# Kernel optimization log

Measured on AMD Instinct MI355X. Metric: run time of the kernel, lower is better.

Reference implementation:

```python
import jax, jax.numpy as jnp
import numpy as np

B, T, C = 4, 2048, 1024
N_HEADS = 16
HEAD_DIM = C // N_HEADS


def rotary_embedding(seq_len, dim, dtype=jnp.float32):
    pos = jnp.arange(seq_len, dtype=dtype)[:, None]
    i = jnp.arange(0, dim, 2, dtype=dtype)[None, :]
    theta = pos / jnp.power(10000.0, i / dim)
    return jnp.cos(theta), jnp.sin(theta)


def apply_rotary(x, cos, sin):
    # x: [B, T, H, D]; cos/sin: [T, D//2]
    d = x.shape[-1]
    x1, x2 = x[..., : d // 2], x[..., d // 2 :]
    rotated = jnp.concatenate([-x2, x1], axis=-1)
    cos = jnp.concatenate([cos, cos], axis=-1)[None, :, None, :]
    sin = jnp.concatenate([sin, sin], axis=-1)[None, :, None, :]
    return x * cos + rotated * sin


def setup_inputs() -> dict:
    key = jax.random.key(0)
    k1, k2, k3 = jax.random.split(key, 3)
    x = jax.random.normal(k1, (B, T, C), dtype=jnp.float32)
    # lecun_normal-ish init scale
    w_qkv = jax.random.normal(k2, (C, 3 * C), dtype=jnp.float32) / np.sqrt(C)
    w_out = jax.random.normal(k3, (C, C), dtype=jnp.float32) / np.sqrt(C)
    return {"x": x, "w_qkv": w_qkv, "w_out": w_out}


def reference(x, w_qkv, w_out):
    b, t, c = x.shape
    qkv = jnp.einsum("btc,cd->btd", x, w_qkv)
    q, k, v = jnp.split(qkv, 3, axis=-1)
    q = q.reshape(b, t, N_HEADS, HEAD_DIM)
    k = k.reshape(b, t, N_HEADS, HEAD_DIM)
    v = v.reshape(b, t, N_HEADS, HEAD_DIM)
    cos, sin = rotary_embedding(t, HEAD_DIM, dtype=x.dtype)
    q = apply_rotary(q, cos, sin)
    k = apply_rotary(k, cos, sin)
    scale = jnp.sqrt(jnp.asarray(HEAD_DIM, dtype=x.dtype))
    # scores: [B, H, T, T]
    attn = jnp.einsum("bqhd,bkhd->bhqk", q, k) / scale
    mask = jnp.tril(jnp.ones((t, t), dtype=jnp.bool_))
    attn = jnp.where(mask[None, None, :, :], attn, jnp.asarray(-1e9, dtype=x.dtype))
    attn = jax.nn.softmax(attn, axis=-1)
    out = jnp.einsum("bhqk,bkhd->bqhd", attn, v).reshape(b, t, c)
    return jnp.einsum("btc,cd->btd", out, w_out)
```

## Files before the change

### kernel.cpp

```cpp
#include <hip/hip_runtime.h>
#include <stdint.h>

#define DEVI __device__ __forceinline__

typedef unsigned short ushort_t;
typedef __bf16 bf16x8 __attribute__((ext_vector_type(8)));
typedef float f32x4 __attribute__((ext_vector_type(4)));
typedef unsigned short ushort8 __attribute__((ext_vector_type(8)));
typedef unsigned short u16x4 __attribute__((ext_vector_type(4)));
typedef short s16x4 __attribute__((ext_vector_type(4)));

#define BB 4
#define TT 2048
#define CC 1024
#define NH 16
#define HD 64
#define MM (BB*TT)

DEVI ushort_t f2bf(float f) {
    __bf16 h = (__bf16)f;
    return __builtin_bit_cast(ushort_t, h);
}

typedef const __attribute__((address_space(1))) unsigned int guint_t;
typedef __attribute__((address_space(3))) unsigned int luint_t;

DEVI void gl2lds16(const void* g, void* lds) {
    __builtin_amdgcn_global_load_lds((guint_t*)(uintptr_t)g,
                                     (luint_t*)(unsigned int)(uintptr_t)lds,
                                     16, 0, 0);
}

template <int N> DEVI void waitvm() {
    static_assert(N == 0 || N == 4, "unsupported vmcnt literal");
    if constexpr (N == 0)      asm volatile("s_waitcnt vmcnt(0)" ::: "memory");
    else if constexpr (N == 4) asm volatile("s_waitcnt vmcnt(4)" ::: "memory");
}

#define BARF() do { asm volatile("" ::: "memory"); \
                    __builtin_amdgcn_s_barrier(); \
                    asm volatile("" ::: "memory"); } while (0)
#define LGK0() asm volatile("s_waitcnt lgkmcnt(0)" ::: "memory")

__global__ void cvt_f32_bf16(const float* __restrict__ in,
                             ushort_t* __restrict__ out) {
    int i = blockIdx.x * 256 + threadIdx.x;
    const float4* p = (const float4*)in + (size_t)i * 2;
    float4 a = p[0], b = p[1];
    ushort8 r;
    r[0] = f2bf(a.x); r[1] = f2bf(a.y); r[2] = f2bf(a.z); r[3] = f2bf(a.w);
    r[4] = f2bf(b.x); r[5] = f2bf(b.y); r[6] = f2bf(b.z); r[7] = f2bf(b.w);
    *(ushort8*)(out + (size_t)i * 8) = r;
}

__global__ void transpose_f2b(const float* __restrict__ in,
                              ushort_t* __restrict__ out, int R, int Cc) {
    __shared__ ushort_t tile[32][33];
    int bx = blockIdx.x * 32;
    int by = blockIdx.y * 32;
    int tx = threadIdx.x & 31, ty = threadIdx.x >> 5;
    #pragma unroll
    for (int i = 0; i < 4; i++) {
        int r = ty * 4 + i;
        tile[r][tx] = f2bf(in[(size_t)(by + r) * Cc + bx + tx]);
    }
    __syncthreads();
    #pragma unroll
    for (int i = 0; i < 4; i++) {
        int r = ty * 4 + i;
        out[(size_t)(bx + r) * R + by + tx] = tile[tx][r];
    }
}

__global__ void rope_table(float2* __restrict__ tab) {
    int i = blockIdx.x * 256 + threadIdx.x;
    int t = i >> 5, j = i & 31;
    float inv = exp2f((float)j * -0.41524101186092029f);
    float theta = (float)t * inv;
    float s, c;
    sincosf(theta, &s, &c);
    tab[i] = make_float2(c, s);
}

template <int MODE>
__global__ __launch_bounds__(512, 2) void gemm_bt(
    const ushort_t* __restrict__ A, const ushort_t* __restrict__ Bt,
    float* __restrict__ CoutF,
    ushort_t* __restrict__ Qb, ushort_t* __restrict__ Kb, ushort_t* __restrict__ VbT,
    const float2* __restrict__ rope, int M, int N, int Kd) {
    constexpr int NK = CC / 64;
    (void)M;

    __shared__ __attribute__((aligned(16))) ushort_t As[2][256 * 64];
    __shared__ __attribute__((aligned(16))) ushort_t Bs[2][256 * 64];

    const int tid = threadIdx.x;
    const int w = tid >> 6, l = tid & 63;
    const int lane15 = l & 15, quad = l >> 4;
    const int wm = (w >> 2) * 128;
    const int wn = (w & 3) * 64;

    const int nbn = gridDim.x;
    const int nwg = nbn * gridDim.y;
    const int lid = blockIdx.y * nbn + blockIdx.x;
    const int sid = (lid & 7) * (nwg >> 3) + (lid >> 3);
    const int bn = sid % nbn, bm = sid / nbn;

    const int sr = tid >> 3;
    const int sc = tid & 7;
    const int srcswz = (sc ^ (sr & 7)) * 16;

    auto stA = [&](int buf, int t, int ln) {
        int gr = bm * 256 + ln * 64 + sr;
        size_t e;
        if constexpr (MODE == 2)
            e = (size_t)(gr >> 11) * 2097152 + (size_t)t * 131072
                + (size_t)(gr & (TT - 1)) * 64;
        else
            e = (size_t)gr * (size_t)Kd + (size_t)t * 64;
        gl2lds16((const char*)(A + e) + srcswz,
                 (char*)&As[buf][0] + ln * 8192 + tid * 16);
    };
    auto stB = [&](int buf, int t, int ln) {
        int gr = bn * 256 + ln * 64 + sr;
        size_t e = (size_t)gr * (size_t)Kd + (size_t)t * 64;
        gl2lds16((const char*)(Bt + e) + srcswz,
                 (char*)&Bs[buf][0] + ln * 8192 + tid * 16);
    };

    f32x4 acc[8][4];
    #pragma unroll
    for (int m = 0; m < 8; ++m)
        #pragma unroll
        for (int n = 0; n < 4; ++n)
            acc[m][n] = f32x4{0.f, 0.f, 0.f, 0.f};

    stA(0, 0, 0); stA(0, 0, 1); stA(0, 0, 2); stA(0, 0, 3);
    stB(0, 0, 0); stB(0, 0, 1); stB(0, 0, 2); stB(0, 0, 3);
    stB(1, 1, 0); stB(1, 1, 1); stB(1, 1, 2); stB(1, 1, 3);
    waitvm<4>();
    BARF();

    const int swz = (lane15 & 7) << 4;
    bf16x8 aR[4][2];
    bf16x8 bR[4][2];

#define LDA_H(P, MH)                                                          \
    { _Pragma("unroll") for (int i = 0; i < 4; ++i)                           \
      _Pragma("unroll") for (int kk = 0; kk < 2; ++kk)                        \
        aR[i][kk] = *(const bf16x8*)((const char*)&As[P][0] +                 \
            (wm + MH * 64 + i * 16 + lane15) * 128 +                          \
            ((kk * 64 + quad * 16) ^ swz)); }

#define LDB_H(P, NHF)                                                         \
    { _Pragma("unroll") for (int j = 0; j < 2; ++j)                           \
      _Pragma("unroll") for (int kk = 0; kk < 2; ++kk)                        \
        bR[NHF * 2 + j][kk] = *(const bf16x8*)((const char*)&Bs[P][0] +       \
            (wn + (NHF * 2 + j) * 16 + lane15) * 128 +                        \
            ((kk * 64 + quad * 16) ^ swz)); }

#define MFMA_Q(MH, NHF)                                                       \
    { __builtin_amdgcn_s_setprio(1);                                          \
      _Pragma("unroll") for (int kk = 0; kk < 2; ++kk)                        \
      _Pragma("unroll") for (int i = 0; i < 4; ++i)                           \
      _Pragma("unroll") for (int j = 0; j < 2; ++j)                           \
        acc[MH * 4 + i][NHF * 2 + j] =                                        \
            __builtin_amdgcn_mfma_f32_16x16x32_bf16(                          \
                aR[i][kk], bR[NHF * 2 + j][kk], acc[MH * 4 + i][NHF * 2 + j], \
                0, 0, 0);                                                     \
      __builtin_amdgcn_s_setprio(0); }

    for (int t = 0; t < NK; ++t) {
        const int p = t & 1;
        const bool s1 = (t + 1 < NK), s2 = (t + 2 < NK);
        LDA_H(p, 0);
        LDB_H(p, 0);
        if (s1) { stA(p ^ 1, t + 1, 0); stA(p ^ 1, t + 1, 1); }
        BARF(); LGK0();
        MFMA_Q(0, 0);
        BARF();
        LDB_H(p, 1);
        if (s1) { stA(p ^ 1, t + 1, 2); stA(p ^ 1, t + 1, 3); }
        BARF(); LGK0();
        MFMA_Q(0, 1);
        BARF();
        LDA_H(p, 1);
        if (s2) { stB(p, t + 2, 0); stB(p, t + 2, 1); }
        BARF(); LGK0();
        MFMA_Q(1, 1);
        BARF();
        if (s2) { stB(p, t + 2, 2); stB(p, t + 2, 3); }
        MFMA_Q(1, 0);
        if (s1) {
            if (s2) waitvm<4>();
            else    waitvm<0>();
            BARF();
        }
    }
#undef LDA_H
#undef LDB_H
#undef MFMA_Q

    if constexpr (MODE == 1) {
        const float SCQ = 0.125f * 1.4426950408889634f;
        const int colbase = bn * 256 + wn;
        const int seg = colbase >> 10;
        const int h = (colbase & 1023) >> 6;
        if (seg == 2) {
            __syncthreads();
            ushort_t* scr = ((w & 4) ? &Bs[0][0] : &As[0][0]) + (w & 3) * 2560;
            const int t0 = bm * 256 + wm;
            const int bq = t0 >> 11;
            const int tb = t0 & (TT - 1);
            const size_t obase = (size_t)(bq * NH + h) * (TT * HD);
            #pragma unroll
            for (int hp = 0; hp < 4; ++hp) {
                #pragma unroll
                for (int mp = 0; mp < 2; ++mp) {
                    int m = hp * 2 + mp;
                    #pragma unroll
                    for (int n = 0; n < 4; ++n) {
                        u16x4 v;
                        v[0] = f2bf(acc[m][n][0]);
                        v[1] = f2bf(acc[m][n][1]);
                        v[2] = f2bf(acc[m][n][2]);
                        v[3] = f2bf(acc[m][n][3]);
                        *(u16x4*)&scr[(n * 16 + lane15) * 40 +
                                      mp * 16 + quad * 4] = v;
                    }
                }
                LGK0();
                __builtin_amdgcn_sched_barrier(0);
                #pragma unroll
                for (int i = 0; i < 4; ++i) {
                    int dd = i * 16 + (l >> 2);
                    int tl = (l & 3) * 8;
                    ushort8 vv = *(const ushort8*)&scr[dd * 40 + tl];
                    *(ushort8*)(VbT + obase + (size_t)dd * TT +
                                tb + hp * 32 + tl) = vv;
                }
                if (hp < 3) { LGK0(); __builtin_amdgcn_sched_barrier(0); }
            }
        } else {
            ushort_t* dst = (seg == 0) ? Qb : Kb;
            #pragma unroll
            for (int m = 0; m < 8; ++m) {
                int row0 = bm * 256 + wm + m * 16 + quad * 4;
                #pragma unroll
                for (int r = 0; r < 4; ++r) {
                    int row = row0 + r;
                    int b = row >> 11, t = row & (TT - 1);
                    size_t ob = ((size_t)(b * NH + h) * TT + t) * HD;
                    #pragma unroll
                    for (int n = 0; n < 2; ++n) {
                        int j = n * 16 + lane15;
                        float2 cs = rope[t * 32 + j];
                        float x1 = acc[m][n][r];
                        float x2 = acc[m][n + 2][r];
                        float y1 = x1 * cs.x - x2 * cs.y;
                        float y2 = x2 * cs.x + x1 * cs.y;
                        if (seg == 0) { y1 *= SCQ; y2 *= SCQ; }
                        dst[ob + j]      = f2bf(y1);
                        dst[ob + 32 + j] = f2bf(y2);
                    }
                }
            }
        }
    } else {
        #pragma unroll
        for (int m = 0; m < 8; ++m) {
            #pragma unroll
            for (int r = 0; r < 4; ++r) {
                size_t rb = (size_t)(bm * 256 + wm + m * 16 + quad * 4 + r) * N
                            + bn * 256 + wn;
                #pragma unroll
                for (int n = 0; n < 4; ++n)
                    CoutF[rb + n * 16 + lane15] = acc[m][n][r];
            }
        }
    }
}

__global__ __launch_bounds__(512, 4) void attn_kernel(
    ushort_t* __restrict__ Qb, const ushort_t* __restrict__ Kb,
    const ushort_t* __restrict__ VbT) {
    __shared__ __attribute__((aligned(16))) ushort_t Ks[2][64 * 64];
    __shared__ __attribute__((aligned(16))) ushort_t Vs[2][64 * 64];

    const int tid = threadIdx.x;
    const int w = tid >> 6, l = tid & 63;
    const int lane15 = l & 15, quad = l >> 4;

    const int d = blockIdx.y * gridDim.x + blockIdx.x;
    const int xcd = d & 7, j = d >> 3;
    const int bh = xcd * 8 + (j & 7);
    const int qt = (int)((0x765489AB3210CDEFull >> (4 * (j >> 3))) & 15);
    const size_t base = (size_t)bh * (TT * HD);

    const int sr = tid >> 3;
    const int sd = (tid & 7) * 8;
    const int scol = (sd * 2) ^ ((sr & 7) << 4);
    const ushort_t* kgb = Kb  + base + (size_t)sr * HD + sd;
    const ushort_t* vgb = VbT + base + (size_t)sr * TT + sd;

    const int q0 = qt * 128;
    const int rbase = q0 + w * 16;
    const int ktmax = 2 * qt + 1;

    bf16x8 qf0, qf1;
    {
        const ushort_t* qp = Qb + base + (size_t)(rbase + lane15) * HD + quad * 8;
        qf0 = *(const bf16x8*)qp;
        qf1 = *(const bf16x8*)(qp + 32);
    }

    f32x4 o[4];
    #pragma unroll
    for (int nt = 0; nt < 4; nt++) o[nt] = f32x4{0.f, 0.f, 0.f, 0.f};
    f32x4 lacc = f32x4{0.f, 0.f, 0.f, 0.f};
    float mrow = -INFINITY;

    const s16x4 ONES = {(short)0x3F80, (short)0x3F80,
                        (short)0x3F80, (short)0x3F80};

    const int rsw = (lane15 & 7) << 4;

    ushort8 kr = *(const ushort8*)kgb;
    ushort8 vr = *(const ushort8*)vgb;
    *(ushort8*)((char*)&Ks[0][0] + sr * 128 + scol) = kr;
    *(ushort8*)((char*)&Vs[0][0] + sr * 128 + scol) = vr;
    kr = *(const ushort8*)(kgb + (size_t)64 * HD);
    vr = *(const ushort8*)(vgb + 64);
    __syncthreads();

    for (int kt = 0; kt <= ktmax; kt++) {
        const int buf = kt & 1;
        if (kt < ktmax) {
            *(ushort8*)((char*)&Ks[buf ^ 1][0] + sr * 128 + scol) = kr;
            *(ushort8*)((char*)&Vs[buf ^ 1][0] + sr * 128 + scol) = vr;
        }
        if (kt + 2 <= ktmax) {
            kr = *(const ushort8*)(kgb + (size_t)(kt + 2) * 64 * HD);
            vr = *(const ushort8*)(vgb + (size_t)(kt + 2) * 64);
        }

        if (kt * 64 <= rbase + 15) {
            f32x4 s[4];
            #pragma unroll
            for (int c = 0; c < 4; c++) {
                const char* krow = (const char*)&Ks[buf][0]
                                   + (c * 16 + lane15) * 128;
                bf16x8 k0 = *(const bf16x8*)(krow + ((quad * 16) ^ rsw));
                bf16x8 k1 = *(const bf16x8*)(krow + ((64 + quad * 16) ^ rsw));
                f32x4 z = f32x4{0.f, 0.f, 0.f, 0.f};
                z = __builtin_amdgcn_mfma_f32_16x16x32_bf16(k0, qf0, z, 0, 0, 0);
                s[c] = __builtin_amdgcn_mfma_f32_16x16x32_bf16(k1, qf1, z, 0, 0, 0);
            }

            const int qrow = rbase + lane15;
            if (kt * 64 + 63 > rbase) {
                #pragma unroll
                for (int c = 0; c < 4; c++)
                    #pragma unroll
                    for (int r = 0; r < 4; r++)
                        if (kt * 64 + c * 16 + quad * 4 + r > qrow) s[c][r] = -1e9f;
            }

            float a0 = fmaxf(fmaxf(s[0][0], s[0][1]), s[0][2]);
            float a1 = fmaxf(fmaxf(s[0][3], s[1][0]), s[1][1]);
            float a2 = fmaxf(fmaxf(s[1][2], s[1][3]), s[2][0]);
            float a3 = fmaxf(fmaxf(s[2][1], s[2][2]), s[2][3]);
            float a4 = fmaxf(fmaxf(s[3][0], s[3][1]), s[3][2]);
            float mt = fmaxf(fmaxf(a0, a1), a2);
            mt = fmaxf(fmaxf(mt, a3), fmaxf(a4, s[3][3]));

            if (!__all(mt - mrow <= 8.0f)) {
                float mf = fmaxf(mt, __shfl_xor(mt, 16, 64));
                mf = fmaxf(mf, __shfl_xor(mf, 32, 64));
                float mn = fmaxf(mrow, mf);
                float alpha = __builtin_amdgcn_exp2f(mrow - mn);
                mrow = mn;
                #pragma unroll
                for (int r = 0; r < 4; r++) {
                    float aO = __shfl(alpha, quad * 4 + r, 64);
                    #pragma unroll
                    for (int nt = 0; nt < 4; nt++) o[nt][r] *= aO;
                    lacc[r] *= aO;
                }
            }

            #pragma unroll
            for (int c = 0; c < 4; c++) {
                s16x4 pf;
                #pragma unroll
                for (int r = 0; r < 4; r++)
                    pf[r] = (short)f2bf(__builtin_amdgcn_exp2f(s[c][r] - mrow));
                lacc = __builtin_amdgcn_mfma_f32_16x16x16bf16_1k(
                    pf, ONES, lacc, 0, 0, 0);
                #pragma unroll
                for (int nt = 0; nt < 4; nt++) {
                    s16x4 vf = *(const s16x4*)((const char*)&Vs[buf][0] +
                        (nt * 16 + lane15) * 128 +
                        ((c * 32 + quad * 8) ^ rsw));
                    o[nt] = __builtin_amdgcn_mfma_f32_16x16x16bf16_1k(
                        pf, vf, o[nt], 0, 0, 0);
                }
            }
        }

        if (kt < ktmax) __syncthreads();
    }

    #pragma unroll
    for (int r = 0; r < 4; r++) {
        float lO = 1.0f / lacc[r];
        size_t rb = base + (size_t)(rbase + quad * 4 + r) * HD;
        #pragma unroll
        for (int nt = 0; nt < 4; nt++)
            Qb[rb + nt * 16 + lane15] = f2bf(o[nt][r] * lO);
    }
}

extern "C" void kernel_launch(void* const* d_in, const int* in_sizes, int n_in,
                              void* d_out, int out_size, void* d_ws, size_t ws_size,
                              hipStream_t stream) {
    const float* x    = (const float*)d_in[0];
    const float* wqkv = (const float*)d_in[1];
    const float* wout = (const float*)d_in[2];
    float* out = (float*)d_out;

    char* ws = (char*)d_ws;
    ushort_t* WqkvT = (ushort_t*)(ws);
    ushort_t* WoutT = (ushort_t*)(ws + 6291456);
    float2*   rope  = (float2*)  (ws + 8388608);
    ushort_t* Xb    = (ushort_t*)(ws + 8912896);
    ushort_t* Qb    = (ushort_t*)(ws + 8912896 + 16777216);
    ushort_t* Kb    = (ushort_t*)(ws + 8912896 + 2 * 16777216);
    ushort_t* VbT   = (ushort_t*)(ws + 8912896 + 3 * 16777216);

    cvt_f32_bf16<<<dim3(MM * CC / (256 * 8)), 256, 0, stream>>>(x, Xb);
    transpose_f2b<<<dim3(3 * CC / 32, CC / 32), 256, 0, stream>>>(wqkv, WqkvT, CC, 3 * CC);
    transpose_f2b<<<dim3(CC / 32, CC / 32), 256, 0, stream>>>(wout, WoutT, CC, CC);
    rope_table<<<dim3(256), 256, 0, stream>>>(rope);

    gemm_bt<1><<<dim3(3 * CC / 256, MM / 256), 512, 0, stream>>>(
        Xb, WqkvT, nullptr, Qb, Kb, VbT, rope, MM, 3 * CC, CC);

    attn_kernel<<<dim3(16, BB * NH), 512, 0, stream>>>(Qb, Kb, VbT);

    gemm_bt<2><<<dim3(CC / 256, MM / 256), 512, 0, stream>>>(
        Qb, WoutT, out, nullptr, nullptr, nullptr, nullptr, MM, CC, CC);
}
```

Before: 250.6 us.

## Fuse prep kernels and pair causal attention query tiles per block

Merges the four preprocessing launches (x conversion, two weight transposes, rope table) into one kernel that dispatches on block index, removing launch overhead. The attention kernel now launches half as many blocks, and each block processes two query tiles, qt=15-xq and qt=xq, one after the other. This gives every block the same amount of causal work, so block-level load imbalance from the triangular mask goes away. The cost is fewer concurrent blocks (512 instead of 1024), less parallelism, and an extra barrier between the two segments.

```diff
diff --git a/kernel.cpp b/kernel.cpp
--- a/kernel.cpp
+++ b/kernel.cpp
@@ -42,44 +42,53 @@
                     asm volatile("" ::: "memory"); } while (0)
 #define LGK0() asm volatile("s_waitcnt lgkmcnt(0)" ::: "memory")
 
-__global__ void cvt_f32_bf16(const float* __restrict__ in,
-                             ushort_t* __restrict__ out) {
-    int i = blockIdx.x * 256 + threadIdx.x;
-    const float4* p = (const float4*)in + (size_t)i * 2;
-    float4 a = p[0], b = p[1];
-    ushort8 r;
-    r[0] = f2bf(a.x); r[1] = f2bf(a.y); r[2] = f2bf(a.z); r[3] = f2bf(a.w);
-    r[4] = f2bf(b.x); r[5] = f2bf(b.y); r[6] = f2bf(b.z); r[7] = f2bf(b.w);
-    *(ushort8*)(out + (size_t)i * 8) = r;
-}
-
-__global__ void transpose_f2b(const float* __restrict__ in,
-                              ushort_t* __restrict__ out, int R, int Cc) {
+__global__ __launch_bounds__(256) void prep(
+    const float* __restrict__ x, ushort_t* __restrict__ Xb,
+    const float* __restrict__ wqkv, ushort_t* __restrict__ WqkvT,
+    const float* __restrict__ wout, ushort_t* __restrict__ WoutT,
+    float2* __restrict__ rope) {
     __shared__ ushort_t tile[32][33];
-    int bx = blockIdx.x * 32;
-    int by = blockIdx.y * 32;
-    int tx = threadIdx.x & 31, ty = threadIdx.x >> 5;
-    #pragma unroll
-    for (int i = 0; i < 4; i++) {
-        int r = ty * 4 + i;
-        tile[r][tx] = f2bf(in[(size_t)(by + r) * Cc + bx + tx]);
+    const int b = blockIdx.x, tid = threadIdx.x;
+    if (b < 4096) {
+        int i = b * 256 + tid;
+        const float4* p = (const float4*)x + (size_t)i * 2;
+        float4 a = p[0], c = p[1];
+        ushort8 r;
+        r[0] = f2bf(a.x); r[1] = f2bf(a.y); r[2] = f2bf(a.z); r[3] = f2bf(a.w);
+        r[4] = f2bf(c.x); r[5] = f2bf(c.y); r[6] = f2bf(c.z); r[7] = f2bf(c.w);
+        *(ushort8*)(Xb + (size_t)i * 8) = r;
+    } else if (b < 8192) {
+        const float* in; ushort_t* out; int Cc, bx, by;
+        if (b < 7168) {
+            int b2 = b - 4096;
+            in = wqkv; out = WqkvT; Cc = 3 * CC;
+            bx = (b2 % 96) * 32; by = (b2 / 96) * 32;
+        } else {
+            int b3 = b - 7168;
+            in = wout; out = WoutT; Cc = CC;
+            bx = (b3 & 31) * 32; by = (b3 >> 5) * 32;
+        }
+        int tx = tid & 31, ty = tid >> 5;
+        #pragma unroll
+        for (int i = 0; i < 4; i++) {
+            int r = ty * 4 + i;
+            tile[r][tx] = f2bf(in[(size_t)(by + r) * Cc + bx + tx]);
+        }
+        __syncthreads();
+        #pragma unroll
+        for (int i = 0; i < 4; i++) {
+            int r = ty * 4 + i;
+            out[(size_t)(bx + r) * CC + by + tx] = tile[tx][r];
+        }
+    } else {
+        int i = (b - 8192) * 256 + tid;
+        int t = i >> 5, jj = i & 31;
+        float inv = exp2f((float)jj * -0.41524101186092029f);
+        float theta = (float)t * inv;
+        float s, c;
+        sincosf(theta, &s, &c);
+        rope[i] = make_float2(c, s);
     }
-    __syncthreads();
-    #pragma unroll
-    for (int i = 0; i < 4; i++) {
-        int r = ty * 4 + i;
-        out[(size_t)(bx + r) * R + by + tx] = tile[tx][r];
-    }
-}
-
-__global__ void rope_table(float2* __restrict__ tab) {
-    int i = blockIdx.x * 256 + threadIdx.x;
-    int t = i >> 5, j = i & 31;
-    float inv = exp2f((float)j * -0.41524101186092029f);
-    float theta = (float)t * inv;
-    float s, c;
-    sincosf(theta, &s, &c);
-    tab[i] = make_float2(c, s);
 }
 
 template <int MODE>
@@ -294,7 +303,7 @@
     const int d = blockIdx.y * gridDim.x + blockIdx.x;
     const int xcd = d & 7, j = d >> 3;
     const int bh = xcd * 8 + (j & 7);
-    const int qt = (int)((0x765489AB3210CDEFull >> (4 * (j >> 3))) & 15);
+    const int xq = j >> 3;
     const size_t base = (size_t)bh * (TT * HD);
 
     const int sr = tid >> 3;
@@ -303,121 +312,128 @@
     const ushort_t* kgb = Kb  + base + (size_t)sr * HD + sd;
     const ushort_t* vgb = VbT + base + (size_t)sr * TT + sd;
 
-    const int q0 = qt * 128;
-    const int rbase = q0 + w * 16;
-    const int ktmax = 2 * qt + 1;
-
-    bf16x8 qf0, qf1;
-    {
-        const ushort_t* qp = Qb + base + (size_t)(rbase + lane15) * HD + quad * 8;
-        qf0 = *(const bf16x8*)qp;
-        qf1 = *(const bf16x8*)(qp + 32);
-    }
-
-    f32x4 o[4];
-    #pragma unroll
-    for (int nt = 0; nt < 4; nt++) o[nt] = f32x4{0.f, 0.f, 0.f, 0.f};
-    f32x4 lacc = f32x4{0.f, 0.f, 0.f, 0.f};
-    float mrow = -INFINITY;
-
+    const int rsw = (lane15 & 7) << 4;
     const s16x4 ONES = {(short)0x3F80, (short)0x3F80,
                         (short)0x3F80, (short)0x3F80};
 
-    const int rsw = (lane15 & 7) << 4;
-
-    ushort8 kr = *(const ushort8*)kgb;
-    ushort8 vr = *(const ushort8*)vgb;
-    *(ushort8*)((char*)&Ks[0][0] + sr * 128 + scol) = kr;
-    *(ushort8*)((char*)&Vs[0][0] + sr * 128 + scol) = vr;
-    kr = *(const ushort8*)(kgb + (size_t)64 * HD);
-    vr = *(const ushort8*)(vgb + 64);
-    __syncthreads();
-
-    for (int kt = 0; kt <= ktmax; kt++) {
-        const int buf = kt & 1;
-        if (kt < ktmax) {
-            *(ushort8*)((char*)&Ks[buf ^ 1][0] + sr * 128 + scol) = kr;
-            *(ushort8*)((char*)&Vs[buf ^ 1][0] + sr * 128 + scol) = vr;
-        }
-        if (kt + 2 <= ktmax) {
-            kr = *(const ushort8*)(kgb + (size_t)(kt + 2) * 64 * HD);
-            vr = *(const ushort8*)(vgb + (size_t)(kt + 2) * 64);
-        }
-
-        if (kt * 64 <= rbase + 15) {
-            f32x4 s[4];
+    #pragma unroll 1
+    for (int seg = 0; seg < 2; ++seg) {
+        const int qt = seg ? xq : 15 - xq;
+        const int q0 = qt * 128;
+        const int rbase = q0 + w * 16;
+        const int ktmax = 2 * qt + 1;
+
+        bf16x8 qf0, qf1;
+        {
+            const ushort_t* qp = Qb + base + (size_t)(rbase + lane15) * HD
+                                 + quad * 8;
+            qf0 = *(const bf16x8*)qp;
+            qf1 = *(const bf16x8*)(qp + 32);
+        }
+
+        f32x4 o[4];
+        #pragma unroll
+        for (int nt = 0; nt < 4; nt++) o[nt] = f32x4{0.f, 0.f, 0.f, 0.f};
+        f32x4 lacc = f32x4{0.f, 0.f, 0.f, 0.f};
+        float mrow = -INFINITY;
+
+        if (seg) __syncthreads();
+
+        ushort8 kr = *(const ushort8*)kgb;
+        ushort8 vr = *(const ushort8*)vgb;
+        *(ushort8*)((char*)&Ks[0][0] + sr * 128 + scol) = kr;
+        *(ushort8*)((char*)&Vs[0][0] + sr * 128 + scol) = vr;
+        kr = *(const ushort8*)(kgb + (size_t)64 * HD);
+        vr = *(const ushort8*)(vgb + 64);
+        __syncthreads();
+
+        for (int kt = 0; kt <= ktmax; kt++) {
+            const int buf = kt & 1;
+            if (kt < ktmax) {
+                *(ushort8*)((char*)&Ks[buf ^ 1][0] + sr * 128 + scol) = kr;
+                *(ushort8*)((char*)&Vs[buf ^ 1][0] + sr * 128 + scol) = vr;
+            }
+            if (kt + 2 <= ktmax) {
+                kr = *(const ushort8*)(kgb + (size_t)(kt + 2) * 64 * HD);
+                vr = *(const ushort8*)(vgb + (size_t)(kt + 2) * 64);
+            }
+
+            if (kt * 64 <= rbase + 15) {
+                f32x4 s[4];
+                #pragma unroll
+                for (int c = 0; c < 4; c++) {
+                    const char* krow = (const char*)&Ks[buf][0]
+                                       + (c * 16 + lane15) * 128;
+                    bf16x8 k0 = *(const bf16x8*)(krow + ((quad * 16) ^ rsw));
+                    bf16x8 k1 = *(const bf16x8*)(krow + ((64 + quad * 16) ^ rsw));
+                    f32x4 z = f32x4{0.f, 0.f, 0.f, 0.f};
+                    z = __builtin_amdgcn_mfma_f32_16x16x32_bf16(k0, qf0, z, 0, 0, 0);
+                    s[c] = __builtin_amdgcn_mfma_f32_16x16x32_bf16(k1, qf1, z, 0, 0, 0);
+                }
+
+                const int qrow = rbase + lane15;
+                if (kt * 64 + 63 > rbase) {
+                    #pragma unroll
+                    for (int c = 0; c < 4; c++)
+                        #pragma unroll
+                        for (int r = 0; r < 4; r++)
+                            if (kt * 64 + c * 16 + quad * 4 + r > qrow)
+                                s[c][r] = -1e9f;
+                }
+
+                float a0 = fmaxf(fmaxf(s[0][0], s[0][1]), s[0][2]);
+                float a1 = fmaxf(fmaxf(s[0][3], s[1][0]), s[1][1]);
+                float a2 = fmaxf(fmaxf(s[1][2], s[1][3]), s[2][0]);
+                float a3 = fmaxf(fmaxf(s[2][1], s[2][2]), s[2][3]);
+                float a4 = fmaxf(fmaxf(s[3][0], s[3][1]), s[3][2]);
+                float mt = fmaxf(fmaxf(a0, a1), a2);
+                mt = fmaxf(fmaxf(mt, a3), fmaxf(a4, s[3][3]));
+
+                if (!__all(mt - mrow <= 8.0f)) {
+                    float mf = fmaxf(mt, __shfl_xor(mt, 16, 64));
+                    mf = fmaxf(mf, __shfl_xor(mf, 32, 64));
+                    float mn = fmaxf(mrow, mf);
+                    float alpha = __builtin_amdgcn_exp2f(mrow - mn);
+                    mrow = mn;
+                    #pragma unroll
+                    for (int r = 0; r < 4; r++) {
+                        float aO = __shfl(alpha, quad * 4 + r, 64);
+                        #pragma unroll
+                        for (int nt = 0; nt < 4; nt++) o[nt][r] *= aO;
+                        lacc[r] *= aO;
+                    }
+                }
+
+                #pragma unroll
+                for (int c = 0; c < 4; c++) {
+                    s16x4 pf;
+                    #pragma unroll
+                    for (int r = 0; r < 4; r++)
+                        pf[r] = (short)f2bf(__builtin_amdgcn_exp2f(s[c][r] - mrow));
+                    lacc = __builtin_amdgcn_mfma_f32_16x16x16bf16_1k(
+                        pf, ONES, lacc, 0, 0, 0);
+                    #pragma unroll
+                    for (int nt = 0; nt < 4; nt++) {
+                        s16x4 vf = *(const s16x4*)((const char*)&Vs[buf][0] +
+                            (nt * 16 + lane15) * 128 +
+                            ((c * 32 + quad * 8) ^ rsw));
+                        o[nt] = __builtin_amdgcn_mfma_f32_16x16x16bf16_1k(
+                            pf, vf, o[nt], 0, 0, 0);
+                    }
+                }
+            }
+
+            if (kt < ktmax) __syncthreads();
+        }
+
+        #pragma unroll
+        for (int r = 0; r < 4; r++) {
+            float lO = 1.0f / lacc[r];
+            size_t rb = base + (size_t)(rbase + quad * 4 + r) * HD;
             #pragma unroll
-            for (int c = 0; c < 4; c++) {
-                const char* krow = (const char*)&Ks[buf][0]
-                                   + (c * 16 + lane15) * 128;
-                bf16x8 k0 = *(const bf16x8*)(krow + ((quad * 16) ^ rsw));
-                bf16x8 k1 = *(const bf16x8*)(krow + ((64 + quad * 16) ^ rsw));
-                f32x4 z = f32x4{0.f, 0.f, 0.f, 0.f};
-                z = __builtin_amdgcn_mfma_f32_16x16x32_bf16(k0, qf0, z, 0, 0, 0);
-                s[c] = __builtin_amdgcn_mfma_f32_16x16x32_bf16(k1, qf1, z, 0, 0, 0);
-            }
-
-            const int qrow = rbase + lane15;
-            if (kt * 64 + 63 > rbase) {
-                #pragma unroll
-                for (int c = 0; c < 4; c++)
-                    #pragma unroll
-                    for (int r = 0; r < 4; r++)
-                        if (kt * 64 + c * 16 + quad * 4 + r > qrow) s[c][r] = -1e9f;
-            }
-
-            float a0 = fmaxf(fmaxf(s[0][0], s[0][1]), s[0][2]);
-            float a1 = fmaxf(fmaxf(s[0][3], s[1][0]), s[1][1]);
-            float a2 = fmaxf(fmaxf(s[1][2], s[1][3]), s[2][0]);
-            float a3 = fmaxf(fmaxf(s[2][1], s[2][2]), s[2][3]);
-            float a4 = fmaxf(fmaxf(s[3][0], s[3][1]), s[3][2]);
-            float mt = fmaxf(fmaxf(a0, a1), a2);
-            mt = fmaxf(fmaxf(mt, a3), fmaxf(a4, s[3][3]));
-
-            if (!__all(mt - mrow <= 8.0f)) {
-                float mf = fmaxf(mt, __shfl_xor(mt, 16, 64));
-                mf = fmaxf(mf, __shfl_xor(mf, 32, 64));
-                float mn = fmaxf(mrow, mf);
-                float alpha = __builtin_amdgcn_exp2f(mrow - mn);
-                mrow = mn;
-                #pragma unroll
-                for (int r = 0; r < 4; r++) {
-                    float aO = __shfl(alpha, quad * 4 + r, 64);
-                    #pragma unroll
-                    for (int nt = 0; nt < 4; nt++) o[nt][r] *= aO;
-                    lacc[r] *= aO;
-                }
-            }
-
-            #pragma unroll
-            for (int c = 0; c < 4; c++) {
-                s16x4 pf;
-                #pragma unroll
-                for (int r = 0; r < 4; r++)
-                    pf[r] = (short)f2bf(__builtin_amdgcn_exp2f(s[c][r] - mrow));
-                lacc = __builtin_amdgcn_mfma_f32_16x16x16bf16_1k(
-                    pf, ONES, lacc, 0, 0, 0);
-                #pragma unroll
-                for (int nt = 0; nt < 4; nt++) {
-                    s16x4 vf = *(const s16x4*)((const char*)&Vs[buf][0] +
-                        (nt * 16 + lane15) * 128 +
-                        ((c * 32 + quad * 8) ^ rsw));
-                    o[nt] = __builtin_amdgcn_mfma_f32_16x16x16bf16_1k(
-                        pf, vf, o[nt], 0, 0, 0);
-                }
-            }
-        }
-
-        if (kt < ktmax) __syncthreads();
-    }
-
-    #pragma unroll
-    for (int r = 0; r < 4; r++) {
-        float lO = 1.0f / lacc[r];
-        size_t rb = base + (size_t)(rbase + quad * 4 + r) * HD;
-        #pragma unroll
-        for (int nt = 0; nt < 4; nt++)
-            Qb[rb + nt * 16 + lane15] = f2bf(o[nt][r] * lO);
+            for (int nt = 0; nt < 4; nt++)
+                Qb[rb + nt * 16 + lane15] = f2bf(o[nt][r] * lO);
+        }
     }
 }
 
@@ -438,15 +454,12 @@
     ushort_t* Kb    = (ushort_t*)(ws + 8912896 + 2 * 16777216);
     ushort_t* VbT   = (ushort_t*)(ws + 8912896 + 3 * 16777216);
 
-    cvt_f32_bf16<<<dim3(MM * CC / (256 * 8)), 256, 0, stream>>>(x, Xb);
-    transpose_f2b<<<dim3(3 * CC / 32, CC / 32), 256, 0, stream>>>(wqkv, WqkvT, CC, 3 * CC);
-    transpose_f2b<<<dim3(CC / 32, CC / 32), 256, 0, stream>>>(wout, WoutT, CC, CC);
-    rope_table<<<dim3(256), 256, 0, stream>>>(rope);
+    prep<<<dim3(8448), 256, 0, stream>>>(x, Xb, wqkv, WqkvT, wout, WoutT, rope);
 
     gemm_bt<1><<<dim3(3 * CC / 256, MM / 256), 512, 0, stream>>>(
         Xb, WqkvT, nullptr, Qb, Kb, VbT, rope, MM, 3 * CC, CC);
 
-    attn_kernel<<<dim3(16, BB * NH), 512, 0, stream>>>(Qb, Kb, VbT);
+    attn_kernel<<<dim3(8, BB * NH), 512, 0, stream>>>(Qb, Kb, VbT);
 
     gemm_bt<2><<<dim3(CC / 256, MM / 256), 512, 0, stream>>>(
         Qb, WoutT, out, nullptr, nullptr, nullptr, nullptr, MM, CC, CC);
```

Measured after the change: 241.9 us. -3.5%, faster.
